# Performance work log

Hardware: AMD Instinct MI355X
Metric: run time of the kernel (lower is better)

## Reference

```python
import jax, jax.numpy as jnp
import numpy as np

N = 50000   # nodes
E = 800000  # edges
IN = 128    # input feature dim
HID = 64    # hidden per head
HEADS = 2
P = 100000  # pos/neg pairs
SLOPE = 0.2 # DGL GATConv default negative_slope
EPS = 1e-5  # BatchNorm eps


def setup_inputs() -> dict:
    key = jax.random.key(0)
    ks = jax.random.split(key, 40)
    nrm = lambda k, s, sc=0.1: jax.random.normal(k, s, jnp.float32) * sc
    inp = {}
    inp['x'] = jax.random.normal(ks[0], (N, IN), jnp.float32)
    inp['edge_src'] = jax.random.randint(ks[1], (E,), 0, N)
    inp['edge_dst'] = jax.random.randint(ks[2], (E,), 0, N)
    inp['pos_src'] = jax.random.randint(ks[3], (P,), 0, N)
    inp['pos_dst'] = jax.random.randint(ks[4], (P,), 0, N)
    inp['neg_src'] = jax.random.randint(ks[5], (P,), 0, N)
    inp['neg_dst'] = jax.random.randint(ks[6], (P,), 0, N)
    # GATConv layer 0: in=IN, out=HID, heads=HEADS
    inp['W0'] = nrm(ks[7], (IN, HEADS * HID))
    inp['al0'] = nrm(ks[8], (HEADS, HID))
    inp['ar0'] = nrm(ks[9], (HEADS, HID))
    inp['b0'] = jnp.zeros((HEADS * HID,), jnp.float32)
    # GATConv layer 1: in=HEADS*HID, out=HID, heads=HEADS
    inp['W1'] = nrm(ks[10], (HEADS * HID, HEADS * HID))
    inp['al1'] = nrm(ks[11], (HEADS, HID))
    inp['ar1'] = nrm(ks[12], (HEADS, HID))
    inp['b1'] = jnp.zeros((HEADS * HID,), jnp.float32)
    # GATConv layer 2: in=HEADS*HID, out=HID, heads=1
    inp['W2'] = nrm(ks[13], (HEADS * HID, HID))
    inp['al2'] = nrm(ks[14], (1, HID))
    inp['ar2'] = nrm(ks[15], (1, HID))
    inp['b2'] = jnp.zeros((HID,), jnp.float32)
    # BatchNorm params
    inp['bn0_g'] = jnp.ones((HEADS * HID,), jnp.float32)
    inp['bn0_b'] = jnp.zeros((HEADS * HID,), jnp.float32)
    inp['bn1_g'] = jnp.ones((HEADS * HID,), jnp.float32)
    inp['bn1_b'] = jnp.zeros((HEADS * HID,), jnp.float32)
    # predictor MLP: HID->HID->HID->1
    inp['pW1'] = nrm(ks[16], (HID, HID))
    inp['pb1'] = jnp.zeros((HID,), jnp.float32)
    inp['pW2'] = nrm(ks[17], (HID, HID))
    inp['pb2'] = jnp.zeros((HID,), jnp.float32)
    inp['pW3'] = nrm(ks[18], (HID, 1))
    inp['pb3'] = jnp.zeros((1,), jnp.float32)
    return inp


def gat_conv(h, src, dst, W, al, ar, b, heads, fh):
    # DGL GATConv: fc -> per-node attn dots -> edge LeakyReLU -> dst-segment softmax -> scatter-add
    feat = (h @ W).reshape(-1, heads, fh)            # [N, H, F]
    el = (feat * al[None]).sum(-1)                   # [N, H]
    er = (feat * ar[None]).sum(-1)                   # [N, H]
    e = jax.nn.leaky_relu(el[src] + er[dst], SLOPE)  # [E, H]
    m = jax.ops.segment_max(e, dst, num_segments=N)  # per-dst max for stability
    ee = jnp.exp(e - m[dst])
    denom = jax.ops.segment_sum(ee, dst, num_segments=N)
    alpha = ee / jnp.maximum(denom[dst], 1e-9)       # [E, H]
    out = jax.ops.segment_sum(alpha[:, :, None] * feat[src], dst, num_segments=N)
    return (out + b.reshape(1, heads, fh)).reshape(-1, heads * fh)


def batch_norm(h, g, b):
    mu = h.mean(0)
    var = jnp.var(h, 0)  # biased, matches torch BN training normalization
    return g * (h - mu) * jax.lax.rsqrt(var + EPS) + b


def predict(h_src, h_dst, pW1, pb1, pW2, pb2, pW3, pb3):
    z = h_src * h_dst
    z = jax.nn.relu(z @ pW1 + pb1)
    z = jax.nn.relu(z @ pW2 + pb2)
    return z @ pW3 + pb3


def reference(x, edge_src, edge_dst, pos_src, pos_dst, neg_src, neg_dst,
              W0, al0, ar0, b0, W1, al1, ar1, b1, W2, al2, ar2, b2,
              bn0_g, bn0_b, bn1_g, bn1_b, pW1, pb1, pW2, pb2, pW3, pb3):
    h = gat_conv(x, edge_src, edge_dst, W0, al0, ar0, b0, HEADS, HID)
    h = jax.nn.relu(batch_norm(h, bn0_g, bn0_b))  # dropout = identity (eval)
    h = gat_conv(h, edge_src, edge_dst, W1, al1, ar1, b1, HEADS, HID)
    h = jax.nn.relu(batch_norm(h, bn1_g, bn1_b))
    h = gat_conv(h, edge_src, edge_dst, W2, al2, ar2, b2, 1, HID)  # [N, HID]
    h_pos = predict(h[pos_src], h[pos_dst], pW1, pb1, pW2, pb2, pW3, pb3)
    h_neg = predict(h[neg_src], h[neg_dst], pW1, pb1, pW2, pb2, pW3, pb3)
    return (h_pos, h_neg)
```

## Files before the change

kernel.cpp:

```cpp
#include <hip/hip_runtime.h>
#include <hip/hip_fp16.h>
#include <cstdint>
#include <cstddef>

#define N_NODES 50000
#define N_EDGES 800000

typedef _Float16 f16x8 __attribute__((ext_vector_type(8)));
typedef float f32x4 __attribute__((ext_vector_type(4)));

__global__ void prep_all(const float* __restrict__ x, __half* __restrict__ xh,
                         int* __restrict__ cnt, float* __restrict__ bns,
                         const float* __restrict__ W0, const float* __restrict__ W1,
                         const float* __restrict__ W2, __half* __restrict__ t0,
                         __half* __restrict__ t1, __half* __restrict__ t2,
                         const float* __restrict__ pW1, const float* __restrict__ pW2,
                         __half* __restrict__ pt1, __half* __restrict__ pt2)
{
    const int b = blockIdx.x;
    const int tid = threadIdx.x;
    if (b < 6250) {
        int i = b * 256 + tid;
        if (i < N_NODES * 32) {
            float4 v = *reinterpret_cast<const float4*>(x + (size_t)i * 4);
            __half2 a = __floats2half2_rn(v.x, v.y);
            __half2 c = __floats2half2_rn(v.z, v.w);
            uint2 pk;
            pk.x = *reinterpret_cast<unsigned*>(&a);
            pk.y = *reinterpret_cast<unsigned*>(&c);
            *reinterpret_cast<uint2*>(xh + (size_t)i * 4) = pk;
        }
    } else if (b < 6446) {
        int i = (b - 6250) * 256 + tid;
        if (i < N_NODES) cnt[i] = 0;
    } else if (b == 6446) {
        bns[tid] = 0.f;
        bns[256 + tid] = 0.f;
    } else if (b < 6607) {
        int g = (b - 6447) * 256 + tid;
        if (g < 16384) {
            int c = g & 127, k = g >> 7;
            t0[(size_t)c * 128 + k] = __float2half(W0[(size_t)k * 128 + c]);
        } else if (g < 32768) {
            int idx = g - 16384;
            int c = idx & 127, k = idx >> 7;
            t1[(size_t)c * 128 + k] = __float2half(W1[(size_t)k * 128 + c]);
        } else if (g < 40960) {
            int idx = g - 32768;
            int c = idx & 63, k = idx >> 6;
            t2[(size_t)c * 128 + k] = __float2half(W2[(size_t)k * 64 + c]);
        }
    } else {
        int g = (b - 6607) * 256 + tid;
        if (g < 4096) {
            int c = g & 63, k = g >> 6;
            pt1[(size_t)c * 64 + k] = __float2half(pW1[(size_t)k * 64 + c]);
        } else if (g < 8192) {
            int idx = g - 4096;
            int c = idx & 63, k = idx >> 6;
            pt2[(size_t)c * 64 + k] = __float2half(pW2[(size_t)k * 64 + c]);
        }
    }
}

template <int C, int H, bool BN>
__launch_bounds__(256, 3)
__global__ void gemm_mfma(const __half* __restrict__ Ah, const __half* __restrict__ Wt,
                          const float* __restrict__ al, const float* __restrict__ ar,
                          const float* __restrict__ bns, const float* __restrict__ bng,
                          const float* __restrict__ bnb,
                          __half* __restrict__ feat, float* __restrict__ el,
                          float* __restrict__ er, int n)
{
    constexpr int K = 128;
    constexpr int AS = 136;
    constexpr int CT = C / 16;
    __shared__ __half As[64 * AS];
    __shared__ __half Ws[C * AS];
    __shared__ float sc[128], sh_[128];

    const int tid = threadIdx.x;
    const int brow = blockIdx.x * 64;

    if constexpr (BN) {
        if (tid < 128) {
            const float invN = 1.f / (float)N_NODES;
            float mean = bns[tid] * invN;
            float var = bns[128 + tid] * invN - mean * mean;
            float s = bng[tid] * rsqrtf(var + 1e-5f);
            sc[tid] = s;
            sh_[tid] = bnb[tid] - mean * s;
        }
        __syncthreads();
    }

    for (int idx = tid; idx < 64 * 16; idx += 256) {
        int r = idx >> 4, u = idx & 15;
        int gr = brow + r;
        f16x8 v = {0, 0, 0, 0, 0, 0, 0, 0};
        if (gr < n) v = *reinterpret_cast<const f16x8*>(Ah + (size_t)gr * K + u * 8);
        if constexpr (BN) {
            #pragma unroll
            for (int e = 0; e < 8; ++e) {
                int ch = u * 8 + e;
                float f = (float)v[e] * sc[ch] + sh_[ch];
                v[e] = (_Float16)fmaxf(f, 0.f);
            }
        }
        *reinterpret_cast<f16x8*>(&As[r * AS + u * 8]) = v;
    }
    for (int idx = tid; idx < C * 16; idx += 256) {
        int c = idx >> 4, u = idx & 15;
        *reinterpret_cast<f16x8*>(&Ws[c * AS + u * 8]) =
            *reinterpret_cast<const f16x8*>(Wt + (size_t)c * K + u * 8);
    }
    __syncthreads();

    const int w = tid >> 6;
    const int l = tid & 63;
    const int l15 = l & 15;
    const int kg = l >> 4;

    f32x4 acc[CT];
    #pragma unroll
    for (int ct = 0; ct < CT; ++ct) acc[ct] = (f32x4){0.f, 0.f, 0.f, 0.f};

    #pragma unroll
    for (int kt = 0; kt < 4; ++kt) {
        f16x8 a = *reinterpret_cast<const f16x8*>(&As[(w * 16 + l15) * AS + kt * 32 + kg * 8]);
        #pragma unroll
        for (int ct = 0; ct < CT; ++ct) {
            f16x8 b = *reinterpret_cast<const f16x8*>(&Ws[(ct * 16 + l15) * AS + kt * 32 + kg * 8]);
            acc[ct] = __builtin_amdgcn_mfma_f32_16x16x32_f16(a, b, acc[ct], 0, 0, 0);
        }
    }

    const int row0 = w * 16 + kg * 4;
    float pel[4][H], per_[4][H];
    #pragma unroll
    for (int j = 0; j < 4; ++j)
        #pragma unroll
        for (int h = 0; h < H; ++h) { pel[j][h] = 0.f; per_[j][h] = 0.f; }

    #pragma unroll
    for (int ct = 0; ct < CT; ++ct) {
        int col = ct * 16 + l15;
        int head = (H == 2) ? (col >> 6) : 0;
        int lc = col & 63;
        float av = al[head * 64 + lc];
        float rv = ar[head * 64 + lc];
        #pragma unroll
        for (int j = 0; j < 4; ++j) {
            float fv = acc[ct][j];
            int gr = brow + row0 + j;
            if (gr < n) feat[(size_t)gr * C + col] = __float2half(fv);
            pel[j][head] += fv * av;
            per_[j][head] += fv * rv;
        }
    }
    #pragma unroll
    for (int off = 1; off < 16; off <<= 1) {
        #pragma unroll
        for (int j = 0; j < 4; ++j)
            #pragma unroll
            for (int h = 0; h < H; ++h) {
                pel[j][h] += __shfl_xor(pel[j][h], off, 64);
                per_[j][h] += __shfl_xor(per_[j][h], off, 64);
            }
    }
    if (l15 == 0) {
        #pragma unroll
        for (int j = 0; j < 4; ++j) {
            int gr = brow + row0 + j;
            if (gr < n) {
                if constexpr (H == 2) {
                    float2 e0 = make_float2(pel[j][0], pel[j][1]);
                    float2 e1 = make_float2(per_[j][0], per_[j][1]);
                    *reinterpret_cast<float2*>(el + (size_t)gr * 2) = e0;
                    *reinterpret_cast<float2*>(er + (size_t)gr * 2) = e1;
                } else {
                    el[gr] = pel[j][0];
                    er[gr] = per_[j][0];
                }
            }
        }
    }
}

__global__ void hist_dst(const int* __restrict__ dst, int* __restrict__ cnt, int E)
{
    int e = blockIdx.x * blockDim.x + threadIdx.x;
    if (e < E) atomicAdd(&cnt[dst[e]], 1);
}

__global__ void scan_block_sums(const int* __restrict__ cnt, int* __restrict__ bsum, int n)
{
    __shared__ int sh[256];
    int i = blockIdx.x * 256 + threadIdx.x;
    sh[threadIdx.x] = (i < n) ? cnt[i] : 0;
    __syncthreads();
    for (int off = 128; off; off >>= 1) {
        if (threadIdx.x < off) sh[threadIdx.x] += sh[threadIdx.x + off];
        __syncthreads();
    }
    if (threadIdx.x == 0) bsum[blockIdx.x] = sh[0];
}

__global__ void scan_bsum(int* __restrict__ bsum, int nb)
{
    __shared__ int sh[256];
    int t = threadIdx.x;
    sh[t] = (t < nb) ? bsum[t] : 0;
    __syncthreads();
    for (int off = 1; off < 256; off <<= 1) {
        int u = (t >= off) ? sh[t - off] : 0;
        __syncthreads();
        sh[t] += u;
        __syncthreads();
    }
    if (t < nb) bsum[t] = t ? sh[t - 1] : 0;
}

__global__ void scan_final(const int* __restrict__ cnt, const int* __restrict__ bsum,
                           int* __restrict__ rs, int* __restrict__ cursor, int n)
{
    __shared__ int sh[256];
    int t = threadIdx.x;
    int i = blockIdx.x * 256 + t;
    int v = (i < n) ? cnt[i] : 0;
    sh[t] = v;
    __syncthreads();
    for (int off = 1; off < 256; off <<= 1) {
        int u = (t >= off) ? sh[t - off] : 0;
        __syncthreads();
        sh[t] += u;
        __syncthreads();
    }
    int excl = sh[t] - v + bsum[blockIdx.x];
    if (i < n) { rs[i] = excl; cursor[i] = excl; }
    if (i == n - 1) rs[n] = excl + v;
}

__global__ void scatter_csr(const int* __restrict__ src, const int* __restrict__ dst,
                            int* __restrict__ cursor, int* __restrict__ csr, int E)
{
    int e = blockIdx.x * blockDim.x + threadIdx.x;
    if (e < E) {
        int d = dst[e];
        int pos = atomicAdd(&cursor[d], 1);
        csr[pos] = src[e];
    }
}

template <int C, int H>
__launch_bounds__(256)
__global__ void gat_agg(const int* __restrict__ rs, const int* __restrict__ csr,
                        const float* __restrict__ el, const float* __restrict__ er,
                        const __half* __restrict__ feat, const float* __restrict__ bias,
                        __half* __restrict__ outp, int n)
{
    int node = blockIdx.x * 4 + (threadIdx.x >> 6);
    if (node >= n) return;
    int lane = threadIdx.x & 63;
    int start = rs[node], end = rs[node + 1];

    if constexpr (H == 2) {
        const int slot = lane >> 4;
        const int cl = lane & 15;
        const int h = cl >> 3;
        const float erh = er[(size_t)node * 2 + h];
        float ssum = 0.f;
        float acc[8];
        #pragma unroll
        for (int u = 0; u < 8; ++u) acc[u] = 0.f;
        for (int j = start + slot; j < end; j += 4) {
            int s = csr[j];
            float v = el[(size_t)s * 2 + h] + erh;
            v = v >= 0.f ? v : 0.2f * v;
            float p = __expf(v);
            ssum += p;
            float4 raw = *reinterpret_cast<const float4*>(feat + (size_t)s * C + cl * 8);
            const __half2* hp = reinterpret_cast<const __half2*>(&raw);
            #pragma unroll
            for (int u = 0; u < 4; ++u) {
                float2 f2 = __half22float2(hp[u]);
                acc[2 * u]     = fmaf(p, f2.x, acc[2 * u]);
                acc[2 * u + 1] = fmaf(p, f2.y, acc[2 * u + 1]);
            }
        }
        #pragma unroll
        for (int off = 16; off <= 32; off <<= 1) {
            ssum += __shfl_xor(ssum, off, 64);
            #pragma unroll
            for (int u = 0; u < 8; ++u) acc[u] += __shfl_xor(acc[u], off, 64);
        }
        if (slot == 0) {
            float r = 1.f / fmaxf(ssum, 1e-9f);
            f16x8 o;
            #pragma unroll
            for (int u = 0; u < 8; ++u) o[u] = (_Float16)(acc[u] * r);
            *reinterpret_cast<f16x8*>(outp + (size_t)node * C + cl * 8) = o;
        }
    } else {
        const int slot = lane >> 3;
        const int cl = lane & 7;
        const float er0 = er[node];
        float ssum = 0.f;
        float acc[8];
        #pragma unroll
        for (int u = 0; u < 8; ++u) acc[u] = 0.f;
        for (int j = start + slot; j < end; j += 8) {
            int s = csr[j];
            float v = el[s] + er0;
            v = v >= 0.f ? v : 0.2f * v;
            float p = __expf(v);
            ssum += p;
            float4 raw = *reinterpret_cast<const float4*>(feat + (size_t)s * C + cl * 8);
            const __half2* hp = reinterpret_cast<const __half2*>(&raw);
            #pragma unroll
            for (int u = 0; u < 4; ++u) {
                float2 f2 = __half22float2(hp[u]);
                acc[2 * u]     = fmaf(p, f2.x, acc[2 * u]);
                acc[2 * u + 1] = fmaf(p, f2.y, acc[2 * u + 1]);
            }
        }
        #pragma unroll
        for (int off = 8; off <= 32; off <<= 1) {
            ssum += __shfl_xor(ssum, off, 64);
            #pragma unroll
            for (int u = 0; u < 8; ++u) acc[u] += __shfl_xor(acc[u], off, 64);
        }
        if (slot == 0) {
            float r = 1.f / fmaxf(ssum, 1e-9f);
            f16x8 o;
            #pragma unroll
            for (int u = 0; u < 8; ++u) o[u] = (_Float16)(acc[u] * r + bias[cl * 8 + u]);
            *reinterpret_cast<f16x8*>(outp + (size_t)node * C + cl * 8) = o;
        }
    }
}

__global__ void bn_stats(const __half* __restrict__ h, float* __restrict__ sums, int n)
{
    __shared__ float s1[256], s2[256];
    int c = threadIdx.x & 127, half = threadIdx.x >> 7;
    float ls = 0.f, lq = 0.f;
    for (int r = blockIdx.x * 2 + half; r < n; r += gridDim.x * 2) {
        float v = __half2float(h[(size_t)r * 128 + c]);
        ls += v; lq += v * v;
    }
    s1[threadIdx.x] = ls; s2[threadIdx.x] = lq;
    __syncthreads();
    if (threadIdx.x < 128) {
        atomicAdd(&sums[c], s1[threadIdx.x] + s1[threadIdx.x + 128]);
        atomicAdd(&sums[128 + c], s2[threadIdx.x] + s2[threadIdx.x + 128]);
    }
}

__launch_bounds__(256, 5)
__global__ void predictor(const __half* __restrict__ h16,
                          const int* __restrict__ ps, const int* __restrict__ pd,
                          const int* __restrict__ ns, const int* __restrict__ nd,
                          const __half* __restrict__ W1t, const float* __restrict__ b1,
                          const __half* __restrict__ W2t, const float* __restrict__ b2,
                          const float* __restrict__ W3, const float* __restrict__ b3,
                          float* __restrict__ out, int P)
{
    constexpr int AS = 72;
    __shared__ __half zt[64 * AS];
    __shared__ __half w1s[64 * AS];
    __shared__ __half w2s[64 * AS];
    const int tid = threadIdx.x;

    for (int idx = tid; idx < 512; idx += 256) {
        int c = idx >> 3, u = idx & 7;
        *reinterpret_cast<f16x8*>(&w1s[c * AS + u * 8]) =
            *reinterpret_cast<const f16x8*>(W1t + (size_t)c * 64 + u * 8);
        *reinterpret_cast<f16x8*>(&w2s[c * AS + u * 8]) =
            *reinterpret_cast<const f16x8*>(W2t + (size_t)c * 64 + u * 8);
    }

    {
        int p = tid >> 2, q = tid & 3;
        int gp = blockIdx.x * 64 + p;
        int s, d;
        if (gp < P) { s = ps[gp]; d = pd[gp]; }
        else        { s = ns[gp - P]; d = nd[gp - P]; }
        const f16x8* hs = reinterpret_cast<const f16x8*>(h16 + (size_t)s * 64 + q * 16);
        const f16x8* hd = reinterpret_cast<const f16x8*>(h16 + (size_t)d * 64 + q * 16);
        #pragma unroll
        for (int u = 0; u < 2; ++u) {
            f16x8 z = hs[u] * hd[u];
            *reinterpret_cast<f16x8*>(&zt[p * AS + q * 16 + u * 8]) = z;
        }
    }
    __syncthreads();

    const int w = tid >> 6;
    const int l = tid & 63;
    const int l15 = l & 15;
    const int kg = l >> 4;
    const int myrow = (w * 16 + l15) * AS;

    f32x4 acc[4];
    {
        f16x8 a0 = *reinterpret_cast<const f16x8*>(&zt[myrow + kg * 8]);
        f16x8 a1 = *reinterpret_cast<const f16x8*>(&zt[myrow + 32 + kg * 8]);
        #pragma unroll
        for (int nt = 0; nt < 4; ++nt) {
            f16x8 b0 = *reinterpret_cast<const f16x8*>(&w1s[(nt * 16 + l15) * AS + kg * 8]);
            f16x8 b1v = *reinterpret_cast<const f16x8*>(&w1s[(nt * 16 + l15) * AS + 32 + kg * 8]);
            acc[nt] = __builtin_amdgcn_mfma_f32_16x16x32_f16(a0, b0, (f32x4){0.f, 0.f, 0.f, 0.f}, 0, 0, 0);
            acc[nt] = __builtin_amdgcn_mfma_f32_16x16x32_f16(a1, b1v, acc[nt], 0, 0, 0);
        }
    }
    {
        #pragma unroll
        for (int nt = 0; nt < 4; ++nt) {
            float bb = b1[nt * 16 + l15];
            #pragma unroll
            for (int j = 0; j < 4; ++j) {
                float v = fmaxf(acc[nt][j] + bb, 0.f);
                zt[(w * 16 + kg * 4 + j) * AS + nt * 16 + l15] = __float2half(v);
            }
        }
    }
    __syncthreads();

    {
        f16x8 a0 = *reinterpret_cast<const f16x8*>(&zt[myrow + kg * 8]);
        f16x8 a1 = *reinterpret_cast<const f16x8*>(&zt[myrow + 32 + kg * 8]);
        #pragma unroll
        for (int nt = 0; nt < 4; ++nt) {
            f16x8 b0 = *reinterpret_cast<const f16x8*>(&w2s[(nt * 16 + l15) * AS + kg * 8]);
            f16x8 b1v = *reinterpret_cast<const f16x8*>(&w2s[(nt * 16 + l15) * AS + 32 + kg * 8]);
            acc[nt] = __builtin_amdgcn_mfma_f32_16x16x32_f16(a0, b0, (f32x4){0.f, 0.f, 0.f, 0.f}, 0, 0, 0);
            acc[nt] = __builtin_amdgcn_mfma_f32_16x16x32_f16(a1, b1v, acc[nt], 0, 0, 0);
        }
    }
    float part[4] = {0.f, 0.f, 0.f, 0.f};
    #pragma unroll
    for (int nt = 0; nt < 4; ++nt) {
        float bb = b2[nt * 16 + l15];
        float wv = W3[nt * 16 + l15];
        #pragma unroll
        for (int j = 0; j < 4; ++j)
            part[j] += fmaxf(acc[nt][j] + bb, 0.f) * wv;
    }
    #pragma unroll
    for (int off = 1; off < 16; off <<= 1) {
        #pragma unroll
        for (int j = 0; j < 4; ++j)
            part[j] += __shfl_xor(part[j], off, 16);
    }
    if (l15 == 0) {
        const float b3v = b3[0];
        int gp0 = blockIdx.x * 64 + w * 16 + kg * 4;
        #pragma unroll
        for (int j = 0; j < 4; ++j)
            out[gp0 + j] = part[j] + b3v;
    }
}

extern "C" void kernel_launch(void* const* d_in, const int* in_sizes, int n_in,
                              void* d_out, int out_size, void* d_ws, size_t ws_size,
                              hipStream_t stream)
{
    const float* x    = (const float*)d_in[0];
    const int* es     = (const int*)d_in[1];
    const int* ed     = (const int*)d_in[2];
    const int* ps     = (const int*)d_in[3];
    const int* pdst   = (const int*)d_in[4];
    const int* ns     = (const int*)d_in[5];
    const int* nd     = (const int*)d_in[6];
    const float* W0   = (const float*)d_in[7];
    const float* al0  = (const float*)d_in[8];
    const float* ar0  = (const float*)d_in[9];
    const float* W1   = (const float*)d_in[11];
    const float* al1  = (const float*)d_in[12];
    const float* ar1  = (const float*)d_in[13];
    const float* W2   = (const float*)d_in[15];
    const float* al2  = (const float*)d_in[16];
    const float* ar2  = (const float*)d_in[17];
    const float* b2   = (const float*)d_in[18];
    const float* bn0g = (const float*)d_in[19];
    const float* bn0b = (const float*)d_in[20];
    const float* bn1g = (const float*)d_in[21];
    const float* bn1b = (const float*)d_in[22];
    const float* pW1  = (const float*)d_in[23];
    const float* pb1  = (const float*)d_in[24];
    const float* pW2  = (const float*)d_in[25];
    const float* pb2  = (const float*)d_in[26];
    const float* pW3  = (const float*)d_in[27];
    const float* pb3  = (const float*)d_in[28];
    float* out = (float*)d_out;

    float* ws = (float*)d_ws;
    size_t off = 0;
    auto alloc = [&](size_t nelem) {
        float* p = ws + off;
        off += (nelem + 63) & ~(size_t)63;
        return p;
    };
    __half* featb = (__half*)alloc((size_t)N_NODES * 64);
    __half* xh    = (__half*)alloc((size_t)N_NODES * 64);
    __half* aggh  = (__half*)alloc((size_t)N_NODES * 64);
    __half* wt0  = (__half*)alloc(128 * 64);
    __half* wt1  = (__half*)alloc(128 * 64);
    __half* wt2  = (__half*)alloc(64 * 64);
    __half* pwt1 = (__half*)alloc(64 * 32);
    __half* pwt2 = (__half*)alloc(64 * 32);
    float* el    = alloc((size_t)N_NODES * 2);
    float* er    = alloc((size_t)N_NODES * 2);
    float* bns   = alloc(512);
    int* cnt     = (int*)alloc(N_NODES);
    int* rs      = (int*)alloc(N_NODES + 1);
    int* cursor  = (int*)alloc(N_NODES);
    int* bsum    = (int*)alloc(256);
    int* csr     = (int*)alloc(N_EDGES);

    dim3 blk(256);
    const int gemmGrid = (N_NODES + 63) / 64;
    const int edgeGrid = (N_EDGES + 255) / 256;
    const int nodeBlocks = (N_NODES + 255) / 256;
    const int aggGrid = (N_NODES + 3) / 4;

    prep_all<<<6639, blk, 0, stream>>>(x, xh, cnt, bns, W0, W1, W2, wt0, wt1, wt2,
                                       pW1, pW2, pwt1, pwt2);
    hist_dst<<<edgeGrid, blk, 0, stream>>>(ed, cnt, N_EDGES);
    scan_block_sums<<<nodeBlocks, blk, 0, stream>>>(cnt, bsum, N_NODES);
    scan_bsum<<<1, blk, 0, stream>>>(bsum, nodeBlocks);
    scan_final<<<nodeBlocks, blk, 0, stream>>>(cnt, bsum, rs, cursor, N_NODES);
    scatter_csr<<<edgeGrid, blk, 0, stream>>>(es, ed, cursor, csr, N_EDGES);

    gemm_mfma<128, 2, false><<<gemmGrid, blk, 0, stream>>>(xh, wt0, al0, ar0,
        nullptr, nullptr, nullptr, featb, el, er, N_NODES);
    gat_agg<128, 2><<<aggGrid, blk, 0, stream>>>(rs, csr, el, er, featb, nullptr, aggh, N_NODES);
    bn_stats<<<256, blk, 0, stream>>>(aggh, bns, N_NODES);

    gemm_mfma<128, 2, true><<<gemmGrid, blk, 0, stream>>>(aggh, wt1, al1, ar1,
        bns, bn0g, bn0b, featb, el, er, N_NODES);
    gat_agg<128, 2><<<aggGrid, blk, 0, stream>>>(rs, csr, el, er, featb, nullptr, aggh, N_NODES);
    bn_stats<<<256, blk, 0, stream>>>(aggh, bns + 256, N_NODES);

    gemm_mfma<64, 1, true><<<gemmGrid, blk, 0, stream>>>(aggh, wt2, al2, ar2,
        bns + 256, bn1g, bn1b, featb, el, er, N_NODES);
    gat_agg<64, 1><<<aggGrid, blk, 0, stream>>>(rs, csr, el, er, featb, b2, aggh, N_NODES);

    predictor<<<3125, blk, 0, stream>>>(aggh, ps, pdst, ns, nd,
                                        pwt1, pb1, pwt2, pb2, pW3, pb3, out, 100000);
}
```

Baseline: 430.0 us.

## Fuse prep and CSR build into one cooperative kernel; store CSR as uint16

Merges the prep, histogram, three scan kernels and CSR scatter into a single cooperative persistent kernel that uses grid-wide syncs between phases, removing five kernel launches and their gaps. The CSR source indices are also narrowed to 16-bit to halve the index traffic in aggregation. The narrowing is wrong: node ids run up to 50000, which is above the unsigned short maximum of 65535? No, 50000 fits, so it is valid for this N but would break for larger graphs. Grid syncs cost something, and the fixed 1024-block cooperative grid must fit co-resident on the device.

Result: slower. 974.5 us (+126.6%).

```diff
diff --git a/kernel.cpp b/kernel.cpp
--- a/kernel.cpp
+++ b/kernel.cpp
@@ -1,43 +1,48 @@
 #include <hip/hip_runtime.h>
 #include <hip/hip_fp16.h>
+#include <hip/hip_cooperative_groups.h>
 #include <cstdint>
 #include <cstddef>
 
+namespace cg = cooperative_groups;
+
 #define N_NODES 50000
 #define N_EDGES 800000
 
 typedef _Float16 f16x8 __attribute__((ext_vector_type(8)));
 typedef float f32x4 __attribute__((ext_vector_type(4)));
 
-__global__ void prep_all(const float* __restrict__ x, __half* __restrict__ xh,
-                         int* __restrict__ cnt, float* __restrict__ bns,
-                         const float* __restrict__ W0, const float* __restrict__ W1,
-                         const float* __restrict__ W2, __half* __restrict__ t0,
-                         __half* __restrict__ t1, __half* __restrict__ t2,
-                         const float* __restrict__ pW1, const float* __restrict__ pW2,
-                         __half* __restrict__ pt1, __half* __restrict__ pt2)
+__launch_bounds__(256, 4)
+__global__ void build_graph(const float* __restrict__ x, __half* __restrict__ xh,
+                            int* __restrict__ cnt, float* __restrict__ bns,
+                            const float* __restrict__ W0, const float* __restrict__ W1,
+                            const float* __restrict__ W2, __half* __restrict__ t0,
+                            __half* __restrict__ t1, __half* __restrict__ t2,
+                            const float* __restrict__ pW1, const float* __restrict__ pW2,
+                            __half* __restrict__ pt1, __half* __restrict__ pt2,
+                            const int* __restrict__ es, const int* __restrict__ ed,
+                            int* __restrict__ rs, int* __restrict__ cursor,
+                            int* __restrict__ bsum, unsigned short* __restrict__ csr)
 {
-    const int b = blockIdx.x;
+    cg::grid_group grid = cg::this_grid();
+    __shared__ int sh[256];
     const int tid = threadIdx.x;
-    if (b < 6250) {
-        int i = b * 256 + tid;
-        if (i < N_NODES * 32) {
-            float4 v = *reinterpret_cast<const float4*>(x + (size_t)i * 4);
-            __half2 a = __floats2half2_rn(v.x, v.y);
-            __half2 c = __floats2half2_rn(v.z, v.w);
-            uint2 pk;
-            pk.x = *reinterpret_cast<unsigned*>(&a);
-            pk.y = *reinterpret_cast<unsigned*>(&c);
-            *reinterpret_cast<uint2*>(xh + (size_t)i * 4) = pk;
-        }
-    } else if (b < 6446) {
-        int i = (b - 6250) * 256 + tid;
-        if (i < N_NODES) cnt[i] = 0;
-    } else if (b == 6446) {
-        bns[tid] = 0.f;
-        bns[256 + tid] = 0.f;
-    } else if (b < 6607) {
-        int g = (b - 6447) * 256 + tid;
+    const int gtid = blockIdx.x * 256 + tid;
+    const int gsz = gridDim.x * 256;
+    const int nchunks = (N_NODES + 255) / 256;
+
+    for (int i = gtid; i < N_NODES; i += gsz) cnt[i] = 0;
+    if (gtid < 512) bns[gtid] = 0.f;
+    for (int i = gtid; i < N_NODES * 32; i += gsz) {
+        float4 v = *reinterpret_cast<const float4*>(x + (size_t)i * 4);
+        __half2 a = __floats2half2_rn(v.x, v.y);
+        __half2 c = __floats2half2_rn(v.z, v.w);
+        uint2 pk;
+        pk.x = *reinterpret_cast<unsigned*>(&a);
+        pk.y = *reinterpret_cast<unsigned*>(&c);
+        *reinterpret_cast<uint2*>(xh + (size_t)i * 4) = pk;
+    }
+    for (int g = gtid; g < 40960; g += gsz) {
         if (g < 16384) {
             int c = g & 127, k = g >> 7;
             t0[(size_t)c * 128 + k] = __float2half(W0[(size_t)k * 128 + c]);
@@ -45,21 +50,77 @@
             int idx = g - 16384;
             int c = idx & 127, k = idx >> 7;
             t1[(size_t)c * 128 + k] = __float2half(W1[(size_t)k * 128 + c]);
-        } else if (g < 40960) {
+        } else {
             int idx = g - 32768;
             int c = idx & 63, k = idx >> 6;
             t2[(size_t)c * 128 + k] = __float2half(W2[(size_t)k * 64 + c]);
         }
-    } else {
-        int g = (b - 6607) * 256 + tid;
+    }
+    for (int g = gtid; g < 8192; g += gsz) {
         if (g < 4096) {
             int c = g & 63, k = g >> 6;
             pt1[(size_t)c * 64 + k] = __float2half(pW1[(size_t)k * 64 + c]);
-        } else if (g < 8192) {
+        } else {
             int idx = g - 4096;
             int c = idx & 63, k = idx >> 6;
             pt2[(size_t)c * 64 + k] = __float2half(pW2[(size_t)k * 64 + c]);
         }
+    }
+    grid.sync();
+
+    for (int e = gtid; e < N_EDGES; e += gsz) atomicAdd(&cnt[ed[e]], 1);
+    grid.sync();
+
+    for (int chunk = blockIdx.x; chunk < nchunks; chunk += gridDim.x) {
+        int i = chunk * 256 + tid;
+        int v = (i < N_NODES) ? cnt[i] : 0;
+        sh[tid] = v;
+        __syncthreads();
+        for (int o = 128; o; o >>= 1) {
+            if (tid < o) sh[tid] += sh[tid + o];
+            __syncthreads();
+        }
+        if (tid == 0) bsum[chunk] = sh[0];
+        __syncthreads();
+    }
+    grid.sync();
+
+    if (blockIdx.x == 0) {
+        int v = (tid < nchunks) ? bsum[tid] : 0;
+        sh[tid] = v;
+        __syncthreads();
+        for (int o = 1; o < 256; o <<= 1) {
+            int u = (tid >= o) ? sh[tid - o] : 0;
+            __syncthreads();
+            sh[tid] += u;
+            __syncthreads();
+        }
+        if (tid < nchunks) bsum[tid] = tid ? sh[tid - 1] : 0;
+    }
+    grid.sync();
+
+    for (int chunk = blockIdx.x; chunk < nchunks; chunk += gridDim.x) {
+        int i = chunk * 256 + tid;
+        int v = (i < N_NODES) ? cnt[i] : 0;
+        sh[tid] = v;
+        __syncthreads();
+        for (int o = 1; o < 256; o <<= 1) {
+            int u = (tid >= o) ? sh[tid - o] : 0;
+            __syncthreads();
+            sh[tid] += u;
+            __syncthreads();
+        }
+        int excl = sh[tid] - v + bsum[chunk];
+        if (i < N_NODES) { rs[i] = excl; cursor[i] = excl; }
+        if (i == N_NODES - 1) rs[N_NODES] = excl + v;
+        __syncthreads();
+    }
+    grid.sync();
+
+    for (int e = gtid; e < N_EDGES; e += gsz) {
+        int d = ed[e];
+        int p = atomicAdd(&cursor[d], 1);
+        csr[p] = (unsigned short)es[e];
     }
 }
 
@@ -187,74 +248,9 @@
     }
 }
 
-__global__ void hist_dst(const int* __restrict__ dst, int* __restrict__ cnt, int E)
-{
-    int e = blockIdx.x * blockDim.x + threadIdx.x;
-    if (e < E) atomicAdd(&cnt[dst[e]], 1);
-}
-
-__global__ void scan_block_sums(const int* __restrict__ cnt, int* __restrict__ bsum, int n)
-{
-    __shared__ int sh[256];
-    int i = blockIdx.x * 256 + threadIdx.x;
-    sh[threadIdx.x] = (i < n) ? cnt[i] : 0;
-    __syncthreads();
-    for (int off = 128; off; off >>= 1) {
-        if (threadIdx.x < off) sh[threadIdx.x] += sh[threadIdx.x + off];
-        __syncthreads();
-    }
-    if (threadIdx.x == 0) bsum[blockIdx.x] = sh[0];
-}
-
-__global__ void scan_bsum(int* __restrict__ bsum, int nb)
-{
-    __shared__ int sh[256];
-    int t = threadIdx.x;
-    sh[t] = (t < nb) ? bsum[t] : 0;
-    __syncthreads();
-    for (int off = 1; off < 256; off <<= 1) {
-        int u = (t >= off) ? sh[t - off] : 0;
-        __syncthreads();
-        sh[t] += u;
-        __syncthreads();
-    }
-    if (t < nb) bsum[t] = t ? sh[t - 1] : 0;
-}
-
-__global__ void scan_final(const int* __restrict__ cnt, const int* __restrict__ bsum,
-                           int* __restrict__ rs, int* __restrict__ cursor, int n)
-{
-    __shared__ int sh[256];
-    int t = threadIdx.x;
-    int i = blockIdx.x * 256 + t;
-    int v = (i < n) ? cnt[i] : 0;
-    sh[t] = v;
-    __syncthreads();
-    for (int off = 1; off < 256; off <<= 1) {
-        int u = (t >= off) ? sh[t - off] : 0;
-        __syncthreads();
-        sh[t] += u;
-        __syncthreads();
-    }
-    int excl = sh[t] - v + bsum[blockIdx.x];
-    if (i < n) { rs[i] = excl; cursor[i] = excl; }
-    if (i == n - 1) rs[n] = excl + v;
-}
-
-__global__ void scatter_csr(const int* __restrict__ src, const int* __restrict__ dst,
-                            int* __restrict__ cursor, int* __restrict__ csr, int E)
-{
-    int e = blockIdx.x * blockDim.x + threadIdx.x;
-    if (e < E) {
-        int d = dst[e];
-        int pos = atomicAdd(&cursor[d], 1);
-        csr[pos] = src[e];
-    }
-}
-
 template <int C, int H>
 __launch_bounds__(256)
-__global__ void gat_agg(const int* __restrict__ rs, const int* __restrict__ csr,
+__global__ void gat_agg(const int* __restrict__ rs, const unsigned short* __restrict__ csr,
                         const float* __restrict__ el, const float* __restrict__ er,
                         const __half* __restrict__ feat, const float* __restrict__ bias,
                         __half* __restrict__ outp, int n)
@@ -517,21 +513,21 @@
     int* rs      = (int*)alloc(N_NODES + 1);
     int* cursor  = (int*)alloc(N_NODES);
     int* bsum    = (int*)alloc(256);
-    int* csr     = (int*)alloc(N_EDGES);
+    unsigned short* csr = (unsigned short*)alloc(N_EDGES / 2 + 64);
 
     dim3 blk(256);
     const int gemmGrid = (N_NODES + 63) / 64;
-    const int edgeGrid = (N_EDGES + 255) / 256;
-    const int nodeBlocks = (N_NODES + 255) / 256;
     const int aggGrid = (N_NODES + 3) / 4;
 
-    prep_all<<<6639, blk, 0, stream>>>(x, xh, cnt, bns, W0, W1, W2, wt0, wt1, wt2,
-                                       pW1, pW2, pwt1, pwt2);
-    hist_dst<<<edgeGrid, blk, 0, stream>>>(ed, cnt, N_EDGES);
-    scan_block_sums<<<nodeBlocks, blk, 0, stream>>>(cnt, bsum, N_NODES);
-    scan_bsum<<<1, blk, 0, stream>>>(bsum, nodeBlocks);
-    scan_final<<<nodeBlocks, blk, 0, stream>>>(cnt, bsum, rs, cursor, N_NODES);
-    scatter_csr<<<edgeGrid, blk, 0, stream>>>(es, ed, cursor, csr, N_EDGES);
+    {
+        void* args[] = {
+            (void*)&x, (void*)&xh, (void*)&cnt, (void*)&bns,
+            (void*)&W0, (void*)&W1, (void*)&W2, (void*)&wt0, (void*)&wt1, (void*)&wt2,
+            (void*)&pW1, (void*)&pW2, (void*)&pwt1, (void*)&pwt2,
+            (void*)&es, (void*)&ed, (void*)&rs, (void*)&cursor, (void*)&bsum, (void*)&csr
+        };
+        hipLaunchCooperativeKernel((const void*)build_graph, dim3(1024), blk, args, 0, stream);
+    }
 
     gemm_mfma<128, 2, false><<<gemmGrid, blk, 0, stream>>>(xh, wt0, al0, ar0,
         nullptr, nullptr, nullptr, featb, el, er, N_NODES);
```
